# Performance work log

Measured on AMD Instinct MI355X. Metric: run time of the kernel, lower is better.

Reference implementation:

```python
import jax, jax.numpy as jnp
import numpy as np

M_TIME = 64      # signal model output length (time points)
N_DICT = 20000   # dictionary entries
B_VOX = 8192     # voxels / batch


def setup_inputs() -> dict:
    key = jax.random.key(0)
    k = jax.random.split(key, 6)
    input_real = jax.random.normal(k[0], (M_TIME, B_VOX), jnp.float32)
    input_imag = jax.random.normal(k[1], (M_TIME, B_VOX), jnp.float32)
    # raw dictionary signals, then normalize columns as append() does
    yr = jax.random.normal(k[2], (M_TIME, N_DICT), jnp.float32)
    yi = jax.random.normal(k[3], (M_TIME, N_DICT), jnp.float32)
    norm = jnp.sqrt(jnp.sum(yr * yr + yi * yi, axis=0))  # (N,)
    inverse_norm_y = 1.0 / norm
    y_real = yr * inverse_norm_y
    y_imag = yi * inverse_norm_y
    x_t1 = jax.random.uniform(k[4], (N_DICT,), jnp.float32, 0.1, 3.0)
    x_t2 = jax.random.uniform(k[5], (N_DICT,), jnp.float32, 0.01, 0.5)
    return {
        'input_real': input_real, 'input_imag': input_imag,
        'y_real': y_real, 'y_imag': y_imag,
        'inverse_norm_y': inverse_norm_y, 'x_t1': x_t1, 'x_t2': x_t2,
    }


def reference(input_real, input_imag, y_real, y_imag, inverse_norm_y, x_t1, x_t2):
    # |<y_n, s_b>|^2 for complex y and complex input, via 4 real GEMMs (as in the
    # original module): sim[n, b]
    sim = (jnp.einsum('mb,mn->nb', input_real, y_real) ** 2
           + jnp.einsum('mb,mn->nb', input_real, y_imag) ** 2
           + jnp.einsum('mb,mn->nb', input_imag, y_real) ** 2
           + jnp.einsum('mb,mn->nb', input_imag, y_imag) ** 2)
    idx = jnp.argmax(sim, axis=0)  # (B,)
    # scale = sum_m conj(y[:, idx]) * input * inverse_norm_y[idx]
    yr = y_real[:, idx]   # (M, B)
    yi = y_imag[:, idx]   # (M, B)
    inv = inverse_norm_y[idx]  # (B,)
    scale_r = jnp.sum(yr * input_real + yi * input_imag, axis=0) * inv
    scale_i = jnp.sum(yr * input_imag - yi * input_real, axis=0) * inv
    # returns (scale, t1, t2) with complex scale split into real/imag, stacked (4, B)
    return jnp.stack([scale_r, scale_i, x_t1[idx], x_t2[idx]])
```

## Files before the change

### kernel.cpp

```cpp
#include <hip/hip_runtime.h>
#include <hip/hip_bf16.h>
#include <stdint.h>

#define M_TIME 64
#define N_DICT 20000
#define B_VOX  8192

#define NTILES 313

typedef _Float16 v8h __attribute__((ext_vector_type(8)));
typedef float    v4f __attribute__((ext_vector_type(4)));
typedef float    v2f __attribute__((ext_vector_type(2)));
typedef __attribute__((address_space(3))) unsigned int  lds_u32;
typedef const __attribute__((address_space(1))) unsigned int glb_u32;

__device__ __forceinline__ unsigned long long u64max(unsigned long long a, unsigned long long b) { return a > b ? a : b; }
__device__ __forceinline__ unsigned umin32(unsigned a, unsigned b) { return a < b ? a : b; }
__device__ __forceinline__ unsigned umax32(unsigned a, unsigned b) { return a > b ? a : b; }
__device__ __forceinline__ unsigned umed3(unsigned a, unsigned b, unsigned c) {
    unsigned d;
    asm("v_med3_u32 %0, %1, %2, %3" : "=v"(d) : "v"(a), "v"(b), "v"(c));
    return d;
}

__global__ __launch_bounds__(256) void split_y(
    const float* __restrict__ yr, const float* __restrict__ yi,
    v8h* __restrict__ yp)
{
    const int u = blockIdx.x * 256 + threadIdx.x;
    const int n_l = u & 63;
    const int j   = (u >> 6) & 7;
    const int T   = (u >> 9) % NTILES;
    const int arr = u / (NTILES * 512);
    if (arr > 1) return;
    const float* P = arr ? yi : yr;
    const int n_g = T * 64 + n_l;
    v8h V;
#pragma unroll
    for (int c = 0; c < 8; ++c) {
        float v = 0.f;
        if (n_g < N_DICT) v = P[(j * 8 + c) * N_DICT + n_g];
        V[c] = (_Float16)v;
    }
    const int fr = (arr * 2 + (j >> 2)) * 4 + (j & 3);
    yp[((size_t)T * 16 + fr) * 64 + n_l] = V;
}

__global__ __launch_bounds__(256) void trans_y(
    const float* __restrict__ yr, const float* __restrict__ yi,
    float2* __restrict__ yt)
{
    __shared__ float tr[64][65];
    __shared__ float ti[64][65];
    const int t  = threadIdx.x;
    const int n0 = blockIdx.x * 64;
    const int nl = t & 63;
    const int mg = t >> 6;
    const bool inb = (n0 + nl) < N_DICT;
#pragma unroll
    for (int i = 0; i < 16; ++i) {
        const int m = mg * 16 + i;
        tr[m][nl] = inb ? yr[m * N_DICT + n0 + nl] : 0.f;
        ti[m][nl] = inb ? yi[m * N_DICT + n0 + nl] : 0.f;
    }
    __syncthreads();
    const int nw = t >> 2;
    const int j  = t & 3;
    if (n0 + nw < N_DICT) {
        float4* dst = (float4*)(yt + (size_t)(n0 + nw) * 64);
#pragma unroll
        for (int k = 0; k < 8; ++k) {
            const int m = j * 16 + 2 * k;
            float4 w;
            w.x = tr[m][nw];     w.y = ti[m][nw];
            w.z = tr[m + 1][nw]; w.w = ti[m + 1][nw];
            dst[j * 8 + k] = w;
        }
    }
}

__global__ __launch_bounds__(256, 2) void gemm_pre(
    const float* __restrict__ ir, const float* __restrict__ ii,
    const v8h* __restrict__ yp,
    unsigned* __restrict__ cand, int tpc, int slots)
{
    __shared__ float4 ys4[3][1024];
    __shared__ unsigned xm[2][2][16][2];

    const int tid  = threadIdx.x;
    const int wave = tid >> 6, lane = tid & 63;
    const int quad = lane >> 4, col = lane & 15;
    const int wb   = wave >> 1, wn = wave & 1;
    const int vox_w = blockIdx.x * 64 + wb * 32;
    const int chunk = blockIdx.y;
    const int T0 = chunk * tpc;
    const int T1 = (T0 + tpc < NTILES) ? T0 + tpc : NTILES;

    auto dma_tile = [&](int T, int buf) {
        const float4* src = (const float4*)((const char*)yp + (size_t)T * 16384);
#pragma unroll
        for (int p = 0; p < 4; ++p) {
            const int base = p * 256 + wave * 64;
            __builtin_amdgcn_global_load_lds(
                (glb_u32*)(src + base + lane),
                (lds_u32*)(&ys4[buf][base]), 16, 0, 0);
        }
    };

    dma_tile(T0, 0);
    if (T0 + 1 < T1) dma_tile(T0 + 1, 1);

    v8h fh[2][2][2];
#pragma unroll
    for (int arr = 0; arr < 2; ++arr) {
        const float* P = arr ? ii : ir;
#pragma unroll
        for (int bt = 0; bt < 2; ++bt) {
            const int b = vox_w + bt * 16 + col;
#pragma unroll
            for (int h = 0; h < 2; ++h) {
                v8h H;
#pragma unroll
                for (int j = 0; j < 8; ++j) {
                    const int k = h * 32 + quad * 8 + j;
                    H[j] = (_Float16)P[k * B_VOX + b];
                }
                fh[arr][bt][h] = H;
            }
        }
    }

    const v4f zc = {0.f, 0.f, 0.f, 0.f};
    unsigned t2a[2] = {0u, 0u}, t2b[2] = {0u, 0u};

    int cur = 0;
    for (int T = T0; T < T1; ++T) {
        if (T + 1 < T1) asm volatile("s_waitcnt vmcnt(4)" ::: "memory");
        else            asm volatile("s_waitcnt vmcnt(0)" ::: "memory");
        __builtin_amdgcn_s_barrier();
        __builtin_amdgcn_sched_barrier(0);
        if (T + 2 < T1) {
            int nb = cur + 2; if (nb >= 3) nb -= 3;
            dma_tile(T + 2, nb);
        }
        const v8h* yv = (const v8h*)ys4[cur];

        v4f acc[2][2][4];
#pragma unroll
        for (int h = 0; h < 2; ++h) {
#pragma unroll
            for (int nt = 0; nt < 2; ++nt) {
                const int nrow = (wn * 2 + nt) * 16 + col;
                const v8h yfr = yv[((0 * 2 + h) * 4 + quad) * 64 + nrow];
                const v8h yfi = yv[((1 * 2 + h) * 4 + quad) * 64 + nrow];
#pragma unroll
                for (int bt = 0; bt < 2; ++bt) {
#define MF(A, B, C) __builtin_amdgcn_mfma_f32_16x16x32_f16(A, B, C, 0, 0, 0)
                    if (h == 0) {
                        acc[bt][nt][0] = MF(yfr, fh[0][bt][0], zc);
                        acc[bt][nt][1] = MF(yfi, fh[0][bt][0], zc);
                        acc[bt][nt][2] = MF(yfr, fh[1][bt][0], zc);
                        acc[bt][nt][3] = MF(yfi, fh[1][bt][0], zc);
                    } else {
                        acc[bt][nt][0] = MF(yfr, fh[0][bt][1], acc[bt][nt][0]);
                        acc[bt][nt][1] = MF(yfi, fh[0][bt][1], acc[bt][nt][1]);
                        acc[bt][nt][2] = MF(yfr, fh[1][bt][1], acc[bt][nt][2]);
                        acc[bt][nt][3] = MF(yfi, fh[1][bt][1], acc[bt][nt][3]);
                    }
#undef MF
                }
            }
        }

        const int tl = T - T0;
#pragma unroll
        for (int nt = 0; nt < 2; ++nt) {
            const unsigned base = 0x1FFFu
                - (unsigned)(tl * 64 + (wn * 2 + nt) * 16 + quad * 4);
            v2f s01[2], s23[2];
#pragma unroll
            for (int bt = 0; bt < 2; ++bt) {
                const v4f a0 = acc[bt][nt][0], a1 = acc[bt][nt][1];
                const v4f a2 = acc[bt][nt][2], a3 = acc[bt][nt][3];
                {
                    const v2f p0 = __builtin_shufflevector(a0, a0, 0, 1);
                    const v2f p1 = __builtin_shufflevector(a1, a1, 0, 1);
                    const v2f p2 = __builtin_shufflevector(a2, a2, 0, 1);
                    const v2f p3 = __builtin_shufflevector(a3, a3, 0, 1);
                    v2f s = p0 * p0;
                    s = __builtin_elementwise_fma(p1, p1, s);
                    s = __builtin_elementwise_fma(p2, p2, s);
                    s = __builtin_elementwise_fma(p3, p3, s);
                    s01[bt] = s;
                }
                {
                    const v2f p0 = __builtin_shufflevector(a0, a0, 2, 3);
                    const v2f p1 = __builtin_shufflevector(a1, a1, 2, 3);
                    const v2f p2 = __builtin_shufflevector(a2, a2, 2, 3);
                    const v2f p3 = __builtin_shufflevector(a3, a3, 2, 3);
                    v2f s = p0 * p0;
                    s = __builtin_elementwise_fma(p1, p1, s);
                    s = __builtin_elementwise_fma(p2, p2, s);
                    s = __builtin_elementwise_fma(p3, p3, s);
                    s23[bt] = s;
                }
            }
#pragma unroll
            for (int r = 0; r < 4; ++r) {
#pragma unroll
                for (int bt = 0; bt < 2; ++bt) {
                    const float s = (r < 2) ? s01[bt][r] : s23[bt][r - 2];
                    const unsigned pb = (__float_as_uint(s) & 0xFFFFE000u)
                                      | (base - (unsigned)r);
                    const unsigned nb = umed3(pb, t2a[bt], t2b[bt]);
                    t2a[bt] = umax32(pb, t2a[bt]);
                    t2b[bt] = nb;
                }
            }
        }
        cur = (cur + 1 == 3) ? 0 : cur + 1;
    }

    unsigned fa1[2], fa2[2];
#pragma unroll
    for (int bt = 0; bt < 2; ++bt) {
        unsigned a1 = t2a[bt], a2 = t2b[bt];
#pragma unroll
        for (int d = 16; d <= 32; d <<= 1) {
            unsigned b1 = (unsigned)__shfl_xor((int)a1, d, 64);
            unsigned b2 = (unsigned)__shfl_xor((int)a2, d, 64);
            unsigned mn = umin32(a1, b1);
            a1 = umax32(a1, b1);
            a2 = umax32(mn, umax32(a2, b2));
        }
        fa1[bt] = a1; fa2[bt] = a2;
    }
    __syncthreads();
    if (wn == 1 && lane < 16) {
#pragma unroll
        for (int bt = 0; bt < 2; ++bt) { xm[wb][bt][lane][0] = fa1[bt]; xm[wb][bt][lane][1] = fa2[bt]; }
    }
    __syncthreads();
    if (wn == 0 && lane < 16) {
#pragma unroll
        for (int bt = 0; bt < 2; ++bt) {
            unsigned b1 = xm[wb][bt][lane][0];
            unsigned b2 = xm[wb][bt][lane][1];
            unsigned m1 = umax32(fa1[bt], b1);
            unsigned m2 = umax32(umin32(fa1[bt], b1), umax32(fa2[bt], b2));
            const size_t vox = vox_w + bt * 16 + lane;
            cand[vox * slots + chunk * 2 + 0] = m1;
            cand[vox * slots + chunk * 2 + 1] = m2;
        }
    }
}

__global__ __launch_bounds__(256) void rescore_finish(
    const float* __restrict__ ir, const float* __restrict__ ii,
    const float* __restrict__ yr, const float* __restrict__ yi,
    const float2* __restrict__ yt,
    const float* __restrict__ inv, const float* __restrict__ x1,
    const float* __restrict__ x2,
    const unsigned* __restrict__ cand, int slots, int tpc,
    float* __restrict__ out)
{
    const int tid  = threadIdx.x;
    const int vox  = blockIdx.x * 4 + (tid >> 6);
    const int slot = tid & 63;

    unsigned p = (slot < slots) ? cand[(size_t)vox * slots + slot] : 0u;
    float sa = __uint_as_float(p & 0xFFFFE000u);
    const int chunkc = slot >> 1;
    const int nn = chunkc * tpc * 64 + (0x1FFF - (int)(p & 0x1FFFu));

    float amax = sa;
#pragma unroll
    for (int d = 1; d <= 32; d <<= 1) amax = fmaxf(amax, __shfl_xor(amax, d, 64));

    unsigned long long q = 0ull;
    float rr = 0.f, ri = 0.f, s1 = 0.f, s2 = 0.f;
    const bool active = (slot < slots) && (nn >= 0) && (nn < N_DICT)
                     && (sa >= 0.97f * amax);
    if (active) {
        if (yt) {
            const float4* yc = (const float4*)(yt + (size_t)nn * 64);
            for (int m2 = 0; m2 < 32; ++m2) {
                const float4 w = yc[m2];
                const int m = 2 * m2;
                float vr0 = ir[m * B_VOX + vox],       vi0 = ii[m * B_VOX + vox];
                float vr1 = ir[(m + 1) * B_VOX + vox], vi1 = ii[(m + 1) * B_VOX + vox];
                rr = fmaf(vr0, w.x, rr); ri = fmaf(vr0, w.y, ri);
                s1 = fmaf(vi0, w.x, s1); s2 = fmaf(vi0, w.y, s2);
                rr = fmaf(vr1, w.z, rr); ri = fmaf(vr1, w.w, ri);
                s1 = fmaf(vi1, w.z, s1); s2 = fmaf(vi1, w.w, s2);
            }
        } else {
            for (int m = 0; m < M_TIME; ++m) {
                float a  = yr[(size_t)m * N_DICT + nn];
                float c  = yi[(size_t)m * N_DICT + nn];
                float vr = ir[m * B_VOX + vox];
                float vi = ii[m * B_VOX + vox];
                rr = fmaf(vr, a, rr); ri = fmaf(vr, c, ri);
                s1 = fmaf(vi, a, s1); s2 = fmaf(vi, c, s2);
            }
        }
        float s = fmaf(rr, rr, fmaf(ri, ri, fmaf(s1, s1, s2 * s2)));
        q = (((unsigned long long)__float_as_uint(s)) << 32)
          | (unsigned long long)(0xFFFFFFFFu - (unsigned)nn);
    }
    unsigned long long qm = q;
#pragma unroll
    for (int d = 1; d <= 32; d <<= 1) qm = u64max(qm, __shfl_xor(qm, d, 64));

    if (active && q == qm && qm != 0ull) {
        float ss = inv[nn];
        out[0 * B_VOX + vox] = (rr + s2) * ss;
        out[1 * B_VOX + vox] = (s1 - ri) * ss;
        out[2 * B_VOX + vox] = x1[nn];
        out[3 * B_VOX + vox] = x2[nn];
    }
}

__global__ __launch_bounds__(256, 3) void argmax_naive(
    const float* __restrict__ ir, const float* __restrict__ ii,
    const float* __restrict__ yr, const float* __restrict__ yi,
    int* __restrict__ idxout)
{
    int b = blockIdx.x * 256 + threadIdx.x;
    float bs = -1.0f; int bn = 0;
    for (int n = 0; n < N_DICT; ++n) {
        float a_rr = 0.f, a_ri = 0.f, a_s1 = 0.f, a_s2 = 0.f;
        for (int m = 0; m < M_TIME; ++m) {
            float a = yr[m * N_DICT + n], c = yi[m * N_DICT + n];
            float vr = ir[m * B_VOX + b], vi = ii[m * B_VOX + b];
            a_rr = fmaf(vr, a, a_rr); a_ri = fmaf(vr, c, a_ri);
            a_s1 = fmaf(vi, a, a_s1); a_s2 = fmaf(vi, c, a_s2);
        }
        float sim = fmaf(a_rr, a_rr, fmaf(a_ri, a_ri, fmaf(a_s1, a_s1, a_s2 * a_s2)));
        if (sim > bs) { bs = sim; bn = n; }
    }
    idxout[b] = bn;
}

__global__ void finish_k(const float* __restrict__ ir, const float* __restrict__ ii,
                         const float* __restrict__ yr, const float* __restrict__ yi,
                         const float* __restrict__ inv, const float* __restrict__ x1,
                         const float* __restrict__ x2,
                         const int* __restrict__ idxin, float* __restrict__ out)
{
    int b = blockIdx.x * blockDim.x + threadIdx.x;
    int idx = idxin[b];
    float ar = 0.f, ai = 0.f;
    for (int m = 0; m < M_TIME; ++m) {
        float a  = yr[(size_t)m * N_DICT + idx];
        float c  = yi[(size_t)m * N_DICT + idx];
        float vr = ir[m * B_VOX + b];
        float vi = ii[m * B_VOX + b];
        ar = fmaf(a, vr, ar); ar = fmaf(c, vi, ar);
        ai = fmaf(a, vi, ai); ai = fmaf(-c, vr, ai);
    }
    float s = inv[idx];
    out[0 * B_VOX + b] = ar * s;
    out[1 * B_VOX + b] = ai * s;
    out[2 * B_VOX + b] = x1[idx];
    out[3 * B_VOX + b] = x2[idx];
}

extern "C" void kernel_launch(void* const* d_in, const int* in_sizes, int n_in,
                              void* d_out, int out_size, void* d_ws, size_t ws_size,
                              hipStream_t stream) {
    const float* ir  = (const float*)d_in[0];
    const float* ii  = (const float*)d_in[1];
    const float* yr  = (const float*)d_in[2];
    const float* yi  = (const float*)d_in[3];
    const float* inv = (const float*)d_in[4];
    const float* x1  = (const float*)d_in[5];
    const float* x2  = (const float*)d_in[6];
    float* out = (float*)d_out;

    const size_t yp_bytes = (size_t)NTILES * 16384;
    const size_t yt_bytes = (size_t)N_DICT * 64 * sizeof(float2);

    int CH = 0; bool use_yt = false;
    for (int c = 32; c >= 4; c >>= 1) {
        size_t cand_bytes = (size_t)B_VOX * (2 * c) * sizeof(unsigned);
        if (ws_size >= cand_bytes + yp_bytes + yt_bytes) { CH = c; use_yt = true; break; }
    }
    if (CH == 0) {
        for (int c = 32; c >= 4; c >>= 1) {
            size_t cand_bytes = (size_t)B_VOX * (2 * c) * sizeof(unsigned);
            if (ws_size >= cand_bytes + yp_bytes) { CH = c; break; }
        }
    }

    if (CH > 0) {
        const int slots = 2 * CH;
        const int tpc   = (NTILES + CH - 1) / CH;
        unsigned* cand = (unsigned*)d_ws;
        v8h* yp = (v8h*)((char*)d_ws + (size_t)B_VOX * slots * sizeof(unsigned));
        float2* yt = use_yt ? (float2*)((char*)yp + yp_bytes) : nullptr;

        const int units = 2 * NTILES * 512;
        split_y<<<(units + 255) / 256, 256, 0, stream>>>(yr, yi, yp);
        if (use_yt) trans_y<<<NTILES, 256, 0, stream>>>(yr, yi, yt);
        gemm_pre<<<dim3(B_VOX / 64, CH), 256, 0, stream>>>(ir, ii, yp, cand, tpc, slots);
        rescore_finish<<<B_VOX / 4, 256, 0, stream>>>(ir, ii, yr, yi, yt, inv, x1, x2,
                                                      cand, slots, tpc, out);
    } else {
        int* idxo = (int*)(out + 3 * B_VOX);
        argmax_naive<<<B_VOX / 256, 256, 0, stream>>>(ir, ii, yr, yi, idxo);
        finish_k<<<B_VOX / 256, 256, 0, stream>>>(ir, ii, yr, yi,
                                                  inv, x1, x2, idxo, out);
    }
}
```

Baseline: 201.3 us.

## Use double-buffered LDS in gemm_pre and add overlapped workspace mode

Shrinks the LDS tile ring in gemm_pre from three buffers to two, aliases the xm scratch array onto the tile buffer, and replaces the explicit vmcnt wait plus raw barrier with __syncthreads and a one-tile-ahead prefetch. This cuts LDS use per block, which may allow more blocks per CU, but it reduces how far loads run ahead of compute. The host adds a mode that places the transposed dictionary in the same workspace region as the packed fp16 tiles and builds it after gemm_pre, for when the workspace cannot hold both. The existing path is still chosen when space allows.

```diff
diff --git a/kernel.cpp b/kernel.cpp
--- a/kernel.cpp
+++ b/kernel.cpp
@@ -84,8 +84,8 @@
     const v8h* __restrict__ yp,
     unsigned* __restrict__ cand, int tpc, int slots)
 {
-    __shared__ float4 ys4[3][1024];
-    __shared__ unsigned xm[2][2][16][2];
+    __shared__ float4 ys4[2][1024];
+    unsigned (*xm)[2][16][2] = (unsigned (*)[2][16][2])&ys4[0][0];
 
     const int tid  = threadIdx.x;
     const int wave = tid >> 6, lane = tid & 63;
@@ -108,7 +108,6 @@
     };
 
     dma_tile(T0, 0);
-    if (T0 + 1 < T1) dma_tile(T0 + 1, 1);
 
     v8h fh[2][2][2];
 #pragma unroll
@@ -133,17 +132,11 @@
     const v4f zc = {0.f, 0.f, 0.f, 0.f};
     unsigned t2a[2] = {0u, 0u}, t2b[2] = {0u, 0u};
 
-    int cur = 0;
     for (int T = T0; T < T1; ++T) {
-        if (T + 1 < T1) asm volatile("s_waitcnt vmcnt(4)" ::: "memory");
-        else            asm volatile("s_waitcnt vmcnt(0)" ::: "memory");
-        __builtin_amdgcn_s_barrier();
-        __builtin_amdgcn_sched_barrier(0);
-        if (T + 2 < T1) {
-            int nb = cur + 2; if (nb >= 3) nb -= 3;
-            dma_tile(T + 2, nb);
-        }
-        const v8h* yv = (const v8h*)ys4[cur];
+        const int par = (T - T0) & 1;
+        __syncthreads();
+        if (T + 1 < T1) dma_tile(T + 1, par ^ 1);
+        const v8h* yv = (const v8h*)ys4[par];
 
         v4f acc[2][2][4];
 #pragma unroll
@@ -218,7 +211,6 @@
                 }
             }
         }
-        cur = (cur + 1 == 3) ? 0 : cur + 1;
     }
 
     unsigned fa1[2], fa2[2];
@@ -380,30 +372,37 @@
 
     const size_t yp_bytes = (size_t)NTILES * 16384;
     const size_t yt_bytes = (size_t)N_DICT * 64 * sizeof(float2);
-
-    int CH = 0; bool use_yt = false;
-    for (int c = 32; c >= 4; c >>= 1) {
-        size_t cand_bytes = (size_t)B_VOX * (2 * c) * sizeof(unsigned);
-        if (ws_size >= cand_bytes + yp_bytes + yt_bytes) { CH = c; use_yt = true; break; }
-    }
-    if (CH == 0) {
-        for (int c = 32; c >= 4; c >>= 1) {
-            size_t cand_bytes = (size_t)B_VOX * (2 * c) * sizeof(unsigned);
-            if (ws_size >= cand_bytes + yp_bytes) { CH = c; break; }
-        }
+    const size_t ov_bytes = yt_bytes > yp_bytes ? yt_bytes : yp_bytes;
+
+    int CH = 0, mode = -1;
+    for (int c = 32; c >= 4 && CH == 0; c >>= 1) {
+        size_t cb = (size_t)B_VOX * (2 * c) * sizeof(unsigned);
+        if (ws_size >= cb + yp_bytes + yt_bytes) { CH = c; mode = 1; }
+    }
+    for (int c = 32; c >= 4 && CH == 0; c >>= 1) {
+        size_t cb = (size_t)B_VOX * (2 * c) * sizeof(unsigned);
+        if (ws_size >= cb + ov_bytes) { CH = c; mode = 2; }
+    }
+    for (int c = 32; c >= 4 && CH == 0; c >>= 1) {
+        size_t cb = (size_t)B_VOX * (2 * c) * sizeof(unsigned);
+        if (ws_size >= cb + yp_bytes) { CH = c; mode = 0; }
     }
 
     if (CH > 0) {
         const int slots = 2 * CH;
         const int tpc   = (NTILES + CH - 1) / CH;
         unsigned* cand = (unsigned*)d_ws;
-        v8h* yp = (v8h*)((char*)d_ws + (size_t)B_VOX * slots * sizeof(unsigned));
-        float2* yt = use_yt ? (float2*)((char*)yp + yp_bytes) : nullptr;
+        char* base = (char*)d_ws + (size_t)B_VOX * slots * sizeof(unsigned);
+        v8h*    yp = (v8h*)base;
+        float2* yt = nullptr;
+        if (mode == 1) yt = (float2*)(base + yp_bytes);
+        if (mode == 2) yt = (float2*)base;
 
         const int units = 2 * NTILES * 512;
         split_y<<<(units + 255) / 256, 256, 0, stream>>>(yr, yi, yp);
-        if (use_yt) trans_y<<<NTILES, 256, 0, stream>>>(yr, yi, yt);
+        if (mode == 1) trans_y<<<NTILES, 256, 0, stream>>>(yr, yi, yt);
         gemm_pre<<<dim3(B_VOX / 64, CH), 256, 0, stream>>>(ir, ii, yp, cand, tpc, slots);
+        if (mode == 2) trans_y<<<NTILES, 256, 0, stream>>>(yr, yi, yt);
         rescore_finish<<<B_VOX / 4, 256, 0, stream>>>(ir, ii, yr, yi, yt, inv, x1, x2,
                                                       cand, slots, tpc, out);
     } else {
```

New measurement: 191.1 us. 5.1% less time.
